# Optimization experiments

Measured on AMD Instinct MI355X. Metric: run time of the kernel, lower is better.

Reference implementation:

```python
import jax, jax.numpy as jnp
import numpy as np

B, N, C, R = 4, 4096, 64, 16
EPS = 1e-12


def setup_inputs() -> dict:
    key = jax.random.key(0)
    k_x, k_w, k_u = jax.random.split(key, 3)
    x = jax.random.normal(k_x, (B, N, C), dtype=jnp.float32)
    W = jax.random.uniform(k_w, (B, N, N), dtype=jnp.float32)
    # lazily-initialized learnable low-rank factor U ~ 0.01 * randn(N, r)
    U = 0.01 * jax.random.normal(k_u, (N, R), dtype=jnp.float32)
    w_scale = jnp.asarray(1.0, dtype=jnp.float32)
    return {"x": x, "W": W, "U": U, "w_scale": w_scale}


def reference(x, W, U, w_scale):
    # symmetrize adjacency: W <- (W + W^T)/2
    Ws = 0.5 * (W + jnp.swapaxes(W, -1, -2))            # [B,N,N]
    # low-rank symmetric gate A = sigmoid(U U^T), shared over batch
    A = jax.nn.sigmoid(U @ U.T)                          # [N,N]
    K = Ws * A[None, :, :]                               # [B,N,N]
    # degree normalization K <- D^{-1/2} K D^{-1/2}
    # (diag_embed + two bmms in the original == row/col broadcast scaling)
    deg = jnp.maximum(K.sum(axis=-1), EPS)               # [B,N]
    d = jax.lax.rsqrt(deg)                               # [B,N]
    K = K * d[:, :, None] * d[:, None, :]                # [B,N,N]
    # coupling: w_scale * K @ x
    return w_scale * jnp.einsum('bnm,bmc->bnc', K, x)    # [B,N,C]
```

## Files before the change

kernel.cpp:

```cpp
#include <hip/hip_runtime.h>
#include <hip/hip_bf16.h>

#define B_ 4
#define N_ 4096
#define C_ 64
#define R_ 16
#define EPS_ 1e-12f

typedef __attribute__((ext_vector_type(8))) short bf16x8;
typedef __attribute__((ext_vector_type(4))) float f32x4;

static __device__ __forceinline__ unsigned short f2bf(float f) {
    unsigned int u = __float_as_uint(f);
    unsigned int r = (u + 0x7fffu + ((u >> 16) & 1u)) >> 16;
    return (unsigned short)r;
}
static __device__ __forceinline__ float bf2f(unsigned short us) {
    return __uint_as_float(((unsigned int)us) << 16);
}

static __device__ __forceinline__ size_t k0f_off(int b, int rt, int k32, int fq, int fr) {
    return ((((size_t)(b * 256 + rt)) * 128 + k32) * 4 + fq) * 128 + fr * 8;
}

__global__ __launch_bounds__(256) void k_pass1(
    const float* __restrict__ W, const float* __restrict__ U,
    unsigned short* __restrict__ K0, float* __restrict__ deg)
{
    const int tj = blockIdx.x, ti = blockIdx.y;
    if (ti > tj) return;
    const int I = ti * 64, J = tj * 64;
    const bool diag = (ti == tj);
    const int t = threadIdx.x;
    const int ii = t >> 2, g = t & 3, jjg = g * 16;

    __shared__ float UJ[64][17];
    __shared__ float Wc[64][65];
    __shared__ __align__(16) unsigned short K0s[64][72];

    {
        const float4 v = *(const float4*)(U + (size_t)(J + (t >> 2)) * R_ + (t & 3) * 4);
        UJ[t >> 2][(t & 3) * 4 + 0] = v.x;
        UJ[t >> 2][(t & 3) * 4 + 1] = v.y;
        UJ[t >> 2][(t & 3) * 4 + 2] = v.z;
        UJ[t >> 2][(t & 3) * 4 + 3] = v.w;
    }

    float4 wcv[4], wrv[4], wcvN[4], wrvN[4];
    #pragma unroll
    for (int k = 0; k < 4; k++) {
        const int idx = t + 256 * k, row = idx >> 4, c4 = idx & 15;
        wcv[k] = *(const float4*)(W + ((size_t)(0 * N_ + J + row)) * N_ + I + c4 * 4);
    }
    #pragma unroll
    for (int h = 0; h < 4; h++)
        wrv[h] = *(const float4*)(W + ((size_t)(0 * N_ + I + ii)) * N_ + J + jjg + 4 * h);

    float ui[16];
    {
        const float* up = U + (size_t)(I + ii) * R_;
        #pragma unroll
        for (int h = 0; h < 4; h++) {
            float4 v = *(const float4*)(up + 4 * h);
            ui[4*h] = v.x; ui[4*h+1] = v.y; ui[4*h+2] = v.z; ui[4*h+3] = v.w;
        }
    }
    __syncthreads();

    float a[16];
    #pragma unroll
    for (int q = 0; q < 16; q++) {
        float s = 0.f;
        #pragma unroll
        for (int k = 0; k < 16; k++) s += ui[k] * UJ[jjg + q][k];
        a[q] = 1.0f / (1.0f + __expf(-s));
    }

    #pragma unroll
    for (int k = 0; k < 4; k++) {
        const int idx = t + 256 * k, row = idx >> 4, c4 = idx & 15;
        Wc[row][c4*4+0] = wcv[k].x; Wc[row][c4*4+1] = wcv[k].y;
        Wc[row][c4*4+2] = wcv[k].z; Wc[row][c4*4+3] = wcv[k].w;
    }
    __syncthreads();

    for (int b = 0; b < B_; b++) {
        if (b < B_ - 1) {
            #pragma unroll
            for (int k = 0; k < 4; k++) {
                const int idx = t + 256 * k, row = idx >> 4, c4 = idx & 15;
                wcvN[k] = *(const float4*)(W + ((size_t)((b+1) * N_ + J + row)) * N_ + I + c4 * 4);
            }
            #pragma unroll
            for (int h = 0; h < 4; h++)
                wrvN[h] = *(const float4*)(W + ((size_t)((b+1) * N_ + I + ii)) * N_ + J + jjg + 4 * h);
        }

        const float* wrf = (const float*)wrv;
        float sumI = 0.f;
        unsigned int pk[8];
        #pragma unroll
        for (int q = 0; q < 16; q++) {
            float k0 = 0.5f * (wrf[q] + Wc[jjg + q][ii]) * a[q];
            sumI += k0;
            unsigned short us = f2bf(k0);
            if (q & 1) pk[q >> 1] |= ((unsigned int)us) << 16;
            else       pk[q >> 1] = us;
        }
        *(int4*)(&K0s[ii][jjg])     = make_int4(pk[0], pk[1], pk[2], pk[3]);
        *(int4*)(&K0s[ii][jjg + 8]) = make_int4(pk[4], pk[5], pk[6], pk[7]);
        {
            const int rt  = (I + ii) >> 4, fr = ii & 15;
            const int k32 = (J >> 5) + (g >> 1), fqa = (g & 1) * 2;
            unsigned short* dst = K0 + k0f_off(b, rt, k32, fqa, fr);
            *(int4*)(dst)       = make_int4(pk[0], pk[1], pk[2], pk[3]);
            *(int4*)(dst + 128) = make_int4(pk[4], pk[5], pk[6], pk[7]);
        }
        {
            float s = sumI + __shfl_xor(sumI, 1, 64);
            s += __shfl_xor(s, 2, 64);
            if (g == 0) atomicAdd(deg + b * N_ + I + ii, s);
        }
        __syncthreads();

        if (!diag) {
            const int c2 = t & 31, r8 = t >> 5;
            unsigned int v[8];
            float cs0 = 0.f, cs1 = 0.f;
            #pragma unroll
            for (int k = 0; k < 8; k++) {
                v[k] = *(const unsigned int*)(&K0s[r8 * 8 + k][c2 * 2]);
                cs0 += bf2f((unsigned short)(v[k] & 0xffffu));
                cs1 += bf2f((unsigned short)(v[k] >> 16));
            }
            unsigned int plo[4], phi[4];
            #pragma unroll
            for (int m = 0; m < 4; m++) {
                plo[m] = (v[2*m] & 0xffffu) | (v[2*m+1] << 16);
                phi[m] = (v[2*m] >> 16) | (v[2*m+1] & 0xffff0000u);
            }
            const int rtp  = (J >> 4) + (c2 >> 3), fr0 = (2 * c2) & 15;
            const int k32p = (I >> 5) + (r8 >> 2), fqp = r8 & 3;
            unsigned short* dst0 = K0 + k0f_off(b, rtp, k32p, fqp, fr0);
            *(int4*)(dst0)     = make_int4(plo[0], plo[1], plo[2], plo[3]);
            *(int4*)(dst0 + 8) = make_int4(phi[0], phi[1], phi[2], phi[3]);
            cs0 += __shfl_xor(cs0, 32, 64);
            cs1 += __shfl_xor(cs1, 32, 64);
            if ((t & 32) == 0) {
                atomicAdd(deg + b * N_ + J + 2 * c2,     cs0);
                atomicAdd(deg + b * N_ + J + 2 * c2 + 1, cs1);
            }
        }
        if (b < B_ - 1) {
            #pragma unroll
            for (int k = 0; k < 4; k++) {
                const int idx = t + 256 * k, row = idx >> 4, c4 = idx & 15;
                Wc[row][c4*4+0] = wcvN[k].x; Wc[row][c4*4+1] = wcvN[k].y;
                Wc[row][c4*4+2] = wcvN[k].z; Wc[row][c4*4+3] = wcvN[k].w;
            }
            #pragma unroll
            for (int h = 0; h < 4; h++) wrv[h] = wrvN[h];
            __syncthreads();
        }
    }
}

__global__ __launch_bounds__(256) void k_xdT(
    const float* __restrict__ x, const float* __restrict__ deg,
    unsigned short* __restrict__ xdT)
{
    const int jt = blockIdx.x, b = blockIdx.y;
    const int J = jt * 64, t = threadIdx.x;
    __shared__ float xt[64][69];
    #pragma unroll
    for (int k = 0; k < 4; k++) {
        int idx = t + 256 * k;
        int row = idx >> 4, f4 = idx & 15;
        float d = rsqrtf(fmaxf(deg[b * N_ + J + row], EPS_));
        float4 v = *(const float4*)(x + ((size_t)(b * N_ + J + row)) * C_ + f4 * 4);
        xt[row][f4*4+0] = v.x * d; xt[row][f4*4+1] = v.y * d;
        xt[row][f4*4+2] = v.z * d; xt[row][f4*4+3] = v.w * d;
    }
    __syncthreads();
    #pragma unroll
    for (int p = 0; p < 2; p++) {
        const int linear = p * 256 + t;
        const int k32h = linear >> 8, rem = linear & 255;
        const int cg = rem >> 6, l = rem & 63, fq = l >> 4, fr = l & 15;
        const int c = cg * 16 + fr;
        const int jb = k32h * 32 + fq * 8;
        unsigned int pk[4];
        #pragma unroll
        for (int m = 0; m < 4; m++) {
            pk[m] = (unsigned int)f2bf(xt[jb + 2*m][c]) |
                    ((unsigned int)f2bf(xt[jb + 2*m + 1][c]) << 16);
        }
        unsigned short* dst = xdT +
            (((size_t)(b * 128 + (J >> 5) + k32h)) * 4 + cg) * 512 + l * 8;
        *(int4*)dst = make_int4(pk[0], pk[1], pk[2], pk[3]);
    }
}

__global__ __launch_bounds__(64, 4) void k_gemm(
    const unsigned short* __restrict__ K0, const unsigned short* __restrict__ xdT,
    const float* __restrict__ deg, const float* __restrict__ wsc_p,
    float* __restrict__ out)
{
    const int blk = blockIdx.x, b = blockIdx.y;
    const int rt = blk >> 2, kq = blk & 3;
    const int l = threadIdx.x;

    const unsigned short* Ap = K0  + (size_t)(b * 256 + rt) * 65536
                                   + (size_t)(kq * 32) * 512 + l * 8;
    const unsigned short* Bp = xdT + (size_t)b * 262144
                                   + (size_t)(kq * 32) * 2048 + l * 8;

    f32x4 acc0 = {0.f,0.f,0.f,0.f}, acc1 = {0.f,0.f,0.f,0.f};
    f32x4 acc2 = {0.f,0.f,0.f,0.f}, acc3 = {0.f,0.f,0.f,0.f};

    #pragma unroll 4
    for (int k = 0; k < 32; k++) {
        bf16x8 av = *(const bf16x8*)(Ap + (size_t)k * 512);
        bf16x8 b0 = *(const bf16x8*)(Bp + (size_t)k * 2048);
        bf16x8 b1 = *(const bf16x8*)(Bp + (size_t)k * 2048 + 512);
        bf16x8 b2 = *(const bf16x8*)(Bp + (size_t)k * 2048 + 1024);
        bf16x8 b3 = *(const bf16x8*)(Bp + (size_t)k * 2048 + 1536);
        acc0 = __builtin_amdgcn_mfma_f32_16x16x32_bf16(av, b0, acc0, 0, 0, 0);
        acc1 = __builtin_amdgcn_mfma_f32_16x16x32_bf16(av, b1, acc1, 0, 0, 0);
        acc2 = __builtin_amdgcn_mfma_f32_16x16x32_bf16(av, b2, acc2, 0, 0, 0);
        acc3 = __builtin_amdgcn_mfma_f32_16x16x32_bf16(av, b3, acc3, 0, 0, 0);
    }

    const int fr = l & 15, fq = l >> 4;
    const float wsc = wsc_p[0];
    #pragma unroll
    for (int r = 0; r < 4; r++) {
        const int row = rt * 16 + fq * 4 + r;
        const float sc = wsc * rsqrtf(fmaxf(deg[b * N_ + row], EPS_));
        float* op = out + ((size_t)(b * N_ + row)) * C_;
        atomicAdd(op + fr,      sc * acc0[r]);
        atomicAdd(op + 16 + fr, sc * acc1[r]);
        atomicAdd(op + 32 + fr, sc * acc2[r]);
        atomicAdd(op + 48 + fr, sc * acc3[r]);
    }
}

extern "C" void kernel_launch(void* const* d_in, const int* in_sizes, int n_in,
                              void* d_out, int out_size, void* d_ws, size_t ws_size,
                              hipStream_t stream)
{
    const float* x   = (const float*)d_in[0];
    const float* W   = (const float*)d_in[1];
    const float* U   = (const float*)d_in[2];
    const float* wsc = (const float*)d_in[3];
    float* out = (float*)d_out;

    unsigned short* K0  = (unsigned short*)d_ws;
    float*          deg = (float*)((char*)d_ws + (size_t)B_ * N_ * N_ * 2);
    unsigned short* xdT = (unsigned short*)((char*)deg + (size_t)B_ * N_ * 4);

    hipMemsetAsync(deg, 0, (size_t)B_ * N_ * sizeof(float), stream);
    hipMemsetAsync(out, 0, (size_t)B_ * N_ * C_ * sizeof(float), stream);
    hipLaunchKernelGGL(k_pass1, dim3(64, 64), dim3(256), 0, stream, W, U, K0, deg);
    hipLaunchKernelGGL(k_xdT,  dim3(64, 4),   dim3(256), 0, stream, x, deg, xdT);
    hipLaunchKernelGGL(k_gemm, dim3(1024, 4), dim3(64),  0, stream, K0, xdT, deg, wsc, out);
}
```

Before: 458.3 us.

## Compute mirrored K0 tile directly from both W tiles instead of transposing via LDS

The pass1 kernel now stages both W[I,J] and W[J,I] tiles in shared memory as full tiles. It computes the upper and mirrored lower K0 tiles independently, each with its own sigmoid gate (with the 0.5 folded in). Before, the lower tile was made by transposing the bf16 result through LDS and recomputing column sums from rounded values. This removes the bf16 transpose step and its extra shuffles. In exchange it doubles the gate computation, uses more shared memory, and adds an extra barrier per batch.

```diff
diff --git a/kernel.cpp b/kernel.cpp
--- a/kernel.cpp
+++ b/kernel.cpp
@@ -15,9 +15,6 @@
     unsigned int r = (u + 0x7fffu + ((u >> 16) & 1u)) >> 16;
     return (unsigned short)r;
 }
-static __device__ __forceinline__ float bf2f(unsigned short us) {
-    return __uint_as_float(((unsigned int)us) << 16);
-}
 
 static __device__ __forceinline__ size_t k0f_off(int b, int rt, int k32, int fq, int fr) {
     return ((((size_t)(b * 256 + rt)) * 128 + k32) * 4 + fq) * 128 + fr * 8;
@@ -32,135 +29,139 @@
     const int I = ti * 64, J = tj * 64;
     const bool diag = (ti == tj);
     const int t = threadIdx.x;
-    const int ii = t >> 2, g = t & 3, jjg = g * 16;
-
-    __shared__ float UJ[64][17];
-    __shared__ float Wc[64][65];
-    __shared__ __align__(16) unsigned short K0s[64][72];
+    const int ii = t >> 2, g = t & 3, jq = g * 16;
+
+    __shared__ float UI[64][17], UJ[64][17];
+    __shared__ float W1[64][65];
+    __shared__ float W2[64][65];
 
     {
-        const float4 v = *(const float4*)(U + (size_t)(J + (t >> 2)) * R_ + (t & 3) * 4);
-        UJ[t >> 2][(t & 3) * 4 + 0] = v.x;
-        UJ[t >> 2][(t & 3) * 4 + 1] = v.y;
-        UJ[t >> 2][(t & 3) * 4 + 2] = v.z;
-        UJ[t >> 2][(t & 3) * 4 + 3] = v.w;
-    }
-
-    float4 wcv[4], wrv[4], wcvN[4], wrvN[4];
+        const int row = t >> 2, q4 = t & 3;
+        const float4 vj = *(const float4*)(U + (size_t)(J + row) * R_ + q4 * 4);
+        UJ[row][q4*4+0] = vj.x; UJ[row][q4*4+1] = vj.y;
+        UJ[row][q4*4+2] = vj.z; UJ[row][q4*4+3] = vj.w;
+        const float4 vi = *(const float4*)(U + (size_t)(I + row) * R_ + q4 * 4);
+        UI[row][q4*4+0] = vi.x; UI[row][q4*4+1] = vi.y;
+        UI[row][q4*4+2] = vi.z; UI[row][q4*4+3] = vi.w;
+    }
+
+    float4 w1v[4], w2v[4];
     #pragma unroll
     for (int k = 0; k < 4; k++) {
         const int idx = t + 256 * k, row = idx >> 4, c4 = idx & 15;
-        wcv[k] = *(const float4*)(W + ((size_t)(0 * N_ + J + row)) * N_ + I + c4 * 4);
-    }
-    #pragma unroll
-    for (int h = 0; h < 4; h++)
-        wrv[h] = *(const float4*)(W + ((size_t)(0 * N_ + I + ii)) * N_ + J + jjg + 4 * h);
-
-    float ui[16];
+        w1v[k] = *(const float4*)(W + ((size_t)(I + row)) * N_ + J + c4 * 4);
+    }
+    if (!diag) {
+        #pragma unroll
+        for (int k = 0; k < 4; k++) {
+            const int idx = t + 256 * k, row = idx >> 4, c4 = idx & 15;
+            w2v[k] = *(const float4*)(W + ((size_t)(J + row)) * N_ + I + c4 * 4);
+        }
+    }
+    __syncthreads();
+
+    float a1[16], a2[16];
     {
-        const float* up = U + (size_t)(I + ii) * R_;
-        #pragma unroll
-        for (int h = 0; h < 4; h++) {
-            float4 v = *(const float4*)(up + 4 * h);
-            ui[4*h] = v.x; ui[4*h+1] = v.y; ui[4*h+2] = v.z; ui[4*h+3] = v.w;
-        }
-    }
-    __syncthreads();
-
-    float a[16];
-    #pragma unroll
-    for (int q = 0; q < 16; q++) {
-        float s = 0.f;
-        #pragma unroll
-        for (int k = 0; k < 16; k++) s += ui[k] * UJ[jjg + q][k];
-        a[q] = 1.0f / (1.0f + __expf(-s));
-    }
-
-    #pragma unroll
-    for (int k = 0; k < 4; k++) {
-        const int idx = t + 256 * k, row = idx >> 4, c4 = idx & 15;
-        Wc[row][c4*4+0] = wcv[k].x; Wc[row][c4*4+1] = wcv[k].y;
-        Wc[row][c4*4+2] = wcv[k].z; Wc[row][c4*4+3] = wcv[k].w;
-    }
-    __syncthreads();
+        float u1[16], u2[16];
+        #pragma unroll
+        for (int k2 = 0; k2 < 16; k2++) { u1[k2] = UI[ii][k2]; u2[k2] = UJ[ii][k2]; }
+        #pragma unroll
+        for (int q = 0; q < 16; q++) {
+            float s = 0.f;
+            #pragma unroll
+            for (int k2 = 0; k2 < 16; k2++) s += u1[k2] * UJ[jq + q][k2];
+            a1[q] = 0.5f / (1.0f + __expf(-s));
+        }
+        if (!diag) {
+            #pragma unroll
+            for (int q = 0; q < 16; q++) {
+                float s = 0.f;
+                #pragma unroll
+                for (int k2 = 0; k2 < 16; k2++) s += u2[k2] * UI[jq + q][k2];
+                a2[q] = 0.5f / (1.0f + __expf(-s));
+            }
+        }
+    }
+
+    float (*W2p)[65] = diag ? W1 : W2;
 
     for (int b = 0; b < B_; b++) {
-        if (b < B_ - 1) {
+        if (b) __syncthreads();
+        #pragma unroll
+        for (int k = 0; k < 4; k++) {
+            const int idx = t + 256 * k, row = idx >> 4, c4 = idx & 15;
+            *(float4*)&W1[row][c4 * 4] = w1v[k];
+        }
+        if (!diag) {
             #pragma unroll
             for (int k = 0; k < 4; k++) {
                 const int idx = t + 256 * k, row = idx >> 4, c4 = idx & 15;
-                wcvN[k] = *(const float4*)(W + ((size_t)((b+1) * N_ + J + row)) * N_ + I + c4 * 4);
-            }
-            #pragma unroll
-            for (int h = 0; h < 4; h++)
-                wrvN[h] = *(const float4*)(W + ((size_t)((b+1) * N_ + I + ii)) * N_ + J + jjg + 4 * h);
-        }
-
-        const float* wrf = (const float*)wrv;
-        float sumI = 0.f;
-        unsigned int pk[8];
-        #pragma unroll
-        for (int q = 0; q < 16; q++) {
-            float k0 = 0.5f * (wrf[q] + Wc[jjg + q][ii]) * a[q];
-            sumI += k0;
-            unsigned short us = f2bf(k0);
-            if (q & 1) pk[q >> 1] |= ((unsigned int)us) << 16;
-            else       pk[q >> 1] = us;
-        }
-        *(int4*)(&K0s[ii][jjg])     = make_int4(pk[0], pk[1], pk[2], pk[3]);
-        *(int4*)(&K0s[ii][jjg + 8]) = make_int4(pk[4], pk[5], pk[6], pk[7]);
+                *(float4*)&W2[row][c4 * 4] = w2v[k];
+            }
+        }
+        __syncthreads();
+
+        if (b < B_ - 1) {
+            const float* Wn = W + (size_t)(b + 1) * N_ * N_;
+            #pragma unroll
+            for (int k = 0; k < 4; k++) {
+                const int idx = t + 256 * k, row = idx >> 4, c4 = idx & 15;
+                w1v[k] = *(const float4*)(Wn + ((size_t)(I + row)) * N_ + J + c4 * 4);
+            }
+            if (!diag) {
+                #pragma unroll
+                for (int k = 0; k < 4; k++) {
+                    const int idx = t + 256 * k, row = idx >> 4, c4 = idx & 15;
+                    w2v[k] = *(const float4*)(Wn + ((size_t)(J + row)) * N_ + I + c4 * 4);
+                }
+            }
+        }
+
         {
-            const int rt  = (I + ii) >> 4, fr = ii & 15;
-            const int k32 = (J >> 5) + (g >> 1), fqa = (g & 1) * 2;
-            unsigned short* dst = K0 + k0f_off(b, rt, k32, fqa, fr);
+            float r1[16];
+            #pragma unroll
+            for (int m = 0; m < 4; m++)
+                *(float4*)&r1[4 * m] = *(const float4*)&W1[ii][jq + 4 * m];
+            float s = 0.f;
+            unsigned int pk[8];
+            #pragma unroll
+            for (int q = 0; q < 16; q++) {
+                float k0 = (r1[q] + W2p[jq + q][ii]) * a1[q];
+                s += k0;
+                unsigned short us = f2bf(k0);
+                if (q & 1) pk[q >> 1] |= ((unsigned int)us) << 16;
+                else       pk[q >> 1] = us;
+            }
+            unsigned short* dst = K0 + k0f_off(b, (I + ii) >> 4,
+                                               (J >> 5) + (g >> 1), (g & 1) * 2, ii & 15);
             *(int4*)(dst)       = make_int4(pk[0], pk[1], pk[2], pk[3]);
             *(int4*)(dst + 128) = make_int4(pk[4], pk[5], pk[6], pk[7]);
-        }
-        {
-            float s = sumI + __shfl_xor(sumI, 1, 64);
+            s += __shfl_xor(s, 1, 64);
             s += __shfl_xor(s, 2, 64);
             if (g == 0) atomicAdd(deg + b * N_ + I + ii, s);
         }
-        __syncthreads();
-
         if (!diag) {
-            const int c2 = t & 31, r8 = t >> 5;
-            unsigned int v[8];
-            float cs0 = 0.f, cs1 = 0.f;
-            #pragma unroll
-            for (int k = 0; k < 8; k++) {
-                v[k] = *(const unsigned int*)(&K0s[r8 * 8 + k][c2 * 2]);
-                cs0 += bf2f((unsigned short)(v[k] & 0xffffu));
-                cs1 += bf2f((unsigned short)(v[k] >> 16));
-            }
-            unsigned int plo[4], phi[4];
-            #pragma unroll
-            for (int m = 0; m < 4; m++) {
-                plo[m] = (v[2*m] & 0xffffu) | (v[2*m+1] << 16);
-                phi[m] = (v[2*m] >> 16) | (v[2*m+1] & 0xffff0000u);
-            }
-            const int rtp  = (J >> 4) + (c2 >> 3), fr0 = (2 * c2) & 15;
-            const int k32p = (I >> 5) + (r8 >> 2), fqp = r8 & 3;
-            unsigned short* dst0 = K0 + k0f_off(b, rtp, k32p, fqp, fr0);
-            *(int4*)(dst0)     = make_int4(plo[0], plo[1], plo[2], plo[3]);
-            *(int4*)(dst0 + 8) = make_int4(phi[0], phi[1], phi[2], phi[3]);
-            cs0 += __shfl_xor(cs0, 32, 64);
-            cs1 += __shfl_xor(cs1, 32, 64);
-            if ((t & 32) == 0) {
-                atomicAdd(deg + b * N_ + J + 2 * c2,     cs0);
-                atomicAdd(deg + b * N_ + J + 2 * c2 + 1, cs1);
-            }
-        }
-        if (b < B_ - 1) {
-            #pragma unroll
-            for (int k = 0; k < 4; k++) {
-                const int idx = t + 256 * k, row = idx >> 4, c4 = idx & 15;
-                Wc[row][c4*4+0] = wcvN[k].x; Wc[row][c4*4+1] = wcvN[k].y;
-                Wc[row][c4*4+2] = wcvN[k].z; Wc[row][c4*4+3] = wcvN[k].w;
-            }
-            #pragma unroll
-            for (int h = 0; h < 4; h++) wrv[h] = wrvN[h];
-            __syncthreads();
+            float r2[16];
+            #pragma unroll
+            for (int m = 0; m < 4; m++)
+                *(float4*)&r2[4 * m] = *(const float4*)&W2[ii][jq + 4 * m];
+            float s = 0.f;
+            unsigned int pk[8];
+            #pragma unroll
+            for (int q = 0; q < 16; q++) {
+                float k0 = (r2[q] + W1[jq + q][ii]) * a2[q];
+                s += k0;
+                unsigned short us = f2bf(k0);
+                if (q & 1) pk[q >> 1] |= ((unsigned int)us) << 16;
+                else       pk[q >> 1] = us;
+            }
+            unsigned short* dst = K0 + k0f_off(b, (J + ii) >> 4,
+                                               (I >> 5) + (g >> 1), (g & 1) * 2, ii & 15);
+            *(int4*)(dst)       = make_int4(pk[0], pk[1], pk[2], pk[3]);
+            *(int4*)(dst + 128) = make_int4(pk[4], pk[5], pk[6], pk[7]);
+            s += __shfl_xor(s, 1, 64);
+            s += __shfl_xor(s, 2, 64);
+            if (g == 0) atomicAdd(deg + b * N_ + J + ii, s);
         }
     }
 }
```

Measured after the change: 608.3 us. +32.7%, slower.
